# Optimization experiments

Hardware: AMD Instinct MI355X
Metric: run time of the kernel (lower is better)

## Reference

```python
import jax, jax.numpy as jnp
import numpy as np

IN_DIM = 256
OUT_DIM = 64
N = 8192
ALPHA = 0.2  # LeakyReLU negative slope
NEG_BIG = -9e15


def setup_inputs() -> dict:
    key = jax.random.key(0)
    k_h, k_A, k_W, k_a = jax.random.split(key, 4)
    h = jax.random.normal(k_h, (N, IN_DIM), dtype=jnp.float32)
    A = jax.random.randint(k_A, (N, N), 0, 2, dtype=jnp.int32)
    # xavier_uniform with gain=1.414
    gain = 1.414
    lim_W = gain * np.sqrt(6.0 / (IN_DIM + OUT_DIM))
    W = jax.random.uniform(k_W, (IN_DIM, OUT_DIM), minval=-lim_W, maxval=lim_W, dtype=jnp.float32)
    lim_a = gain * np.sqrt(6.0 / (2 * OUT_DIM + 1))
    a = jax.random.uniform(k_a, (2 * OUT_DIM, 1), minval=-lim_a, maxval=lim_a, dtype=jnp.float32)
    return {"h": h, "A": A, "W": W, "a": a}


def reference(h, A, W, a):
    # Wh: [N, d]
    Wh = h @ W
    # e_ij = leakyrelu([Wh_i || Wh_j] . a) = leakyrelu(Wh_i.a1 + Wh_j.a2)
    # -> avoid the O(N^2 * 2d) concat; compute rank-1 decomposition directly.
    a1 = a[:OUT_DIM, 0]   # [d]
    a2 = a[OUT_DIM:, 0]   # [d]
    f1 = Wh @ a1          # [N] contribution of source node i
    f2 = Wh @ a2          # [N] contribution of target node j
    e = jax.nn.leaky_relu(f1[:, None] + f2[None, :], negative_slope=ALPHA)  # [N, N]
    e = jnp.where(A > 0, e, NEG_BIG)
    attention = jax.nn.softmax(e, axis=1)  # [N, N]
    # dropout=0.0 (eval mode): identity
    h_prime = attention @ Wh               # [N, d]
    return jax.nn.elu(h_prime)             # concat=True -> ELU
```

## Files before the change

kernel.cpp:

```cpp
#include <hip/hip_runtime.h>
#include <math.h>
#include <stdint.h>

#define NV 8192
#define KD 256
#define DD 64
#define ALPHA 0.2f
#define TI 64
#define SPLIT 8
#define BLK 256

typedef _Float16 half8 __attribute__((ext_vector_type(8)));
typedef float floatx4 __attribute__((ext_vector_type(4)));

#define OFF_WHT  0
#define OFF_F1   (DD * NV / 2)
#define OFF_F2   (OFF_F1 + NV)
#define OFF_PACC (OFF_F2 + NV)

__global__ __launch_bounds__(256) void gat_pre(
    const float* __restrict__ h, const float* __restrict__ W,
    const float* __restrict__ a, ushort* __restrict__ whT,
    float* __restrict__ f1, float* __restrict__ f2) {
  __shared__ float hrow[16][KD];
  __shared__ ushort tw[DD][20];
  const int tid = threadIdx.x;
  const int i0 = blockIdx.x * 16;
#pragma unroll
  for (int u = 0; u < 4; ++u) {
    const int idx = tid + u * 256;
    const int row = idx >> 6, col = (idx & 63) * 4;
    *(float4*)&hrow[row][col] = *(const float4*)&h[(long long)(i0 + row) * KD + col];
  }
  __syncthreads();
  const int d = tid & 63;
  const int rg = tid >> 6;
  float wh[4] = {0.f, 0.f, 0.f, 0.f};
#pragma unroll 4
  for (int c = 0; c < KD; ++c) {
    const float wc = W[c * DD + d];
#pragma unroll
    for (int r = 0; r < 4; ++r) wh[r] += hrow[rg * 4 + r][c] * wc;
  }
  const float a1 = a[d], a2 = a[DD + d];
#pragma unroll
  for (int r = 0; r < 4; ++r) {
    float p1 = wh[r] * a1, p2 = wh[r] * a2;
#pragma unroll
    for (int off = 32; off > 0; off >>= 1) {
      p1 += __shfl_down(p1, off);
      p2 += __shfl_down(p2, off);
    }
    if (d == 0) { f1[i0 + rg * 4 + r] = p1; f2[i0 + rg * 4 + r] = p2; }
    union { _Float16 hf; ushort u; } cv;
    cv.hf = (_Float16)wh[r];
    tw[d][rg * 4 + r] = cv.u;
  }
  __syncthreads();
  if (tid < 128) {
    const int dd = tid >> 1, hf = tid & 1;
    *(uint4*)&whT[(long long)dd * NV + i0 + hf * 8] = *(uint4*)&tw[dd][hf * 8];
  }
}

__global__ __launch_bounds__(BLK) __attribute__((amdgpu_waves_per_eu(4, 8)))
void gat_main(
    const int* __restrict__ A, const ushort* __restrict__ whT,
    const float* __restrict__ f1, const float* __restrict__ f2,
    float* __restrict__ pacc, float* __restrict__ pl, int S) {
  __shared__ float f2_lds[NV / SPLIT];
  __shared__ float redf[4];

  const int tid = threadIdx.x;
  const int wave = tid >> 6, lane = tid & 63;
  const int m_ = lane & 15, quad = lane >> 4;
  const int tile = blockIdx.x & 127;
  const int s = blockIdx.x >> 7;
  const int i0 = tile * TI;
  const int jrange = NV / S;
  const int j0 = s * jrange;

  float m = -1e30f;
#pragma unroll
  for (int q = 0; q < NV / BLK; ++q) m = fmaxf(m, f2[tid + q * BLK]);
#pragma unroll
  for (int off = 32; off > 0; off >>= 1) m = fmaxf(m, __shfl_down(m, off));
  if (lane == 0) redf[wave] = m;

  for (int u = tid * 4; u < jrange; u += BLK * 4)
    *(float4*)&f2_lds[u] = *(const float4*)&f2[j0 + u];
  __syncthreads();

  const float mm = fmaxf(fmaxf(redf[0], redf[1]), fmaxf(redf[2], redf[3]));
  const int row = i0 + wave * 16 + m_;
  const float f1r = f1[row];
  const float xm = f1r + mm;
  const float Mr = fmaxf(xm, ALPHA * xm);

  floatx4 acc[4];
#pragma unroll
  for (int nt = 0; nt < 4; ++nt) acc[nt] = (floatx4){0.f, 0.f, 0.f, 0.f};
  float lp = 0.f;

  const int* Arow = A + (long long)row * NV + j0 + quad * 8;
  const ushort* Bb = whT + j0 + quad * 8;

  int4 aC0 = *(const int4*)(Arow);
  int4 aC1 = *(const int4*)(Arow + 4);
  half8 bC[4];
#pragma unroll
  for (int nt = 0; nt < 4; ++nt)
    bC[nt] = *(const half8*)(Bb + (long long)(nt * 16 + m_) * NV);

  for (int kb = 0; kb < jrange; kb += 32) {
    const int nxt = (kb + 32 < jrange) ? kb + 32 : 0;
    int4 aN0 = *(const int4*)(Arow + nxt);
    int4 aN1 = *(const int4*)(Arow + nxt + 4);
    half8 bN[4];
#pragma unroll
    for (int nt = 0; nt < 4; ++nt)
      bN[nt] = *(const half8*)(Bb + (long long)(nt * 16 + m_) * NV + nxt);

    const int kk = kb + quad * 8;
    const float4 q0 = *(const float4*)&f2_lds[kk];
    const float4 q1 = *(const float4*)&f2_lds[kk + 4];

    union { _Float16 hf[8]; half8 v; } wf;
#define WELT(slot, aval, f2val)                                        \
    { float x = f1r + (f2val); x = fmaxf(x, ALPHA * x);                \
      float w = ((aval) > 0) ? __expf(x - Mr) : 0.f;                   \
      wf.hf[slot] = (_Float16)w; lp += (float)wf.hf[slot]; }
    WELT(0, aC0.x, q0.x) WELT(1, aC0.y, q0.y)
    WELT(2, aC0.z, q0.z) WELT(3, aC0.w, q0.w)
    WELT(4, aC1.x, q1.x) WELT(5, aC1.y, q1.y)
    WELT(6, aC1.z, q1.z) WELT(7, aC1.w, q1.w)
#undef WELT

    acc[0] = __builtin_amdgcn_mfma_f32_16x16x32_f16(wf.v, bC[0], acc[0], 0, 0, 0);
    acc[1] = __builtin_amdgcn_mfma_f32_16x16x32_f16(wf.v, bC[1], acc[1], 0, 0, 0);
    acc[2] = __builtin_amdgcn_mfma_f32_16x16x32_f16(wf.v, bC[2], acc[2], 0, 0, 0);
    acc[3] = __builtin_amdgcn_mfma_f32_16x16x32_f16(wf.v, bC[3], acc[3], 0, 0, 0);

    aC0 = aN0; aC1 = aN1;
#pragma unroll
    for (int nt = 0; nt < 4; ++nt) bC[nt] = bN[nt];
  }

  {
    float v = lp;
    v += __shfl_down(v, 32);
    v += __shfl_down(v, 16);
    if (lane < 16) pl[(long long)s * NV + row] = v;
  }

#pragma unroll
  for (int reg = 0; reg < 4; ++reg) {
    const int i = i0 + wave * 16 + quad * 4 + reg;
    const long long base = ((long long)s * NV + i) * DD + m_;
#pragma unroll
    for (int nt = 0; nt < 4; ++nt) pacc[base + 16 * nt] = acc[nt][reg];
  }
}

__global__ __launch_bounds__(256) void gat_fin(const float* __restrict__ pacc,
                                               const float* __restrict__ pl,
                                               float* __restrict__ out, int S) {
  const int idx = blockIdx.x * 256 + threadIdx.x;
  const int i = idx >> 6;
  float sum = 0.f, l = 0.f;
  for (int q = 0; q < S; ++q) sum += pacc[(long long)q * (NV * DD) + idx];
  for (int q = 0; q < S; ++q) l += pl[q * NV + i];
  const float v = sum / l;
  out[idx] = v > 0.f ? v : expm1f(v);
}

extern "C" void kernel_launch(void* const* d_in, const int* in_sizes, int n_in,
                              void* d_out, int out_size, void* d_ws, size_t ws_size,
                              hipStream_t stream) {
  const float* h = (const float*)d_in[0];
  const int* A = (const int*)d_in[1];
  const float* W = (const float*)d_in[2];
  const float* a = (const float*)d_in[3];
  float* out = (float*)d_out;
  float* ws = (float*)d_ws;

  ushort* whT = (ushort*)(ws + OFF_WHT);
  float* f1 = ws + OFF_F1;
  float* f2 = ws + OFF_F2;
  float* pacc = ws + OFF_PACC;

  const int S = SPLIT;
  float* pl = pacc + (size_t)S * NV * DD;

  gat_pre<<<NV / 16, 256, 0, stream>>>(h, W, a, whT, f1, f2);
  gat_main<<<(NV / TI) * S, BLK, 0, stream>>>(A, whT, f1, f2, pacc, pl, S);
  gat_fin<<<NV * DD / 256, 256, 0, stream>>>(pacc, pl, out, S);
}
```

Measured before the change: 456.9 us.

## Compute softmax row sums via extra MFMA with ones, drop register prefetch, raise split

Replaces the per-element scalar accumulation of the softmax denominator with an extra MFMA against a vector of ones, which takes float adds and a cross-lane shuffle reduction off the VALU. It also removes the manual one-iteration-ahead register prefetch of A and Wh tiles, loading them directly each iteration instead. The split-K factor goes from 8 to 16 for more parallelism. The cost is larger partial buffers and more work in the final reduction, and possibly exposed load latency without the prefetch.

```diff
diff --git a/kernel.cpp b/kernel.cpp
--- a/kernel.cpp
+++ b/kernel.cpp
@@ -7,7 +7,7 @@
 #define DD 64
 #define ALPHA 0.2f
 #define TI 64
-#define SPLIT 8
+#define SPLIT 16
 #define BLK 256
 
 typedef _Float16 half8 __attribute__((ext_vector_type(8)));
@@ -97,29 +97,23 @@
   const float xm = f1r + mm;
   const float Mr = fmaxf(xm, ALPHA * xm);
 
-  floatx4 acc[4];
+  floatx4 acc[4], accl;
 #pragma unroll
   for (int nt = 0; nt < 4; ++nt) acc[nt] = (floatx4){0.f, 0.f, 0.f, 0.f};
-  float lp = 0.f;
+  accl = (floatx4){0.f, 0.f, 0.f, 0.f};
+  const half8 ones = {(_Float16)1.f, (_Float16)1.f, (_Float16)1.f, (_Float16)1.f,
+                      (_Float16)1.f, (_Float16)1.f, (_Float16)1.f, (_Float16)1.f};
 
   const int* Arow = A + (long long)row * NV + j0 + quad * 8;
   const ushort* Bb = whT + j0 + quad * 8;
 
-  int4 aC0 = *(const int4*)(Arow);
-  int4 aC1 = *(const int4*)(Arow + 4);
-  half8 bC[4];
-#pragma unroll
-  for (int nt = 0; nt < 4; ++nt)
-    bC[nt] = *(const half8*)(Bb + (long long)(nt * 16 + m_) * NV);
-
   for (int kb = 0; kb < jrange; kb += 32) {
-    const int nxt = (kb + 32 < jrange) ? kb + 32 : 0;
-    int4 aN0 = *(const int4*)(Arow + nxt);
-    int4 aN1 = *(const int4*)(Arow + nxt + 4);
-    half8 bN[4];
-#pragma unroll
-    for (int nt = 0; nt < 4; ++nt)
-      bN[nt] = *(const half8*)(Bb + (long long)(nt * 16 + m_) * NV + nxt);
+    const int4 a0 = *(const int4*)(Arow + kb);
+    const int4 a1 = *(const int4*)(Arow + kb + 4);
+    half8 b0 = *(const half8*)(Bb + (long long)(0 * 16 + m_) * NV + kb);
+    half8 b1 = *(const half8*)(Bb + (long long)(1 * 16 + m_) * NV + kb);
+    half8 b2 = *(const half8*)(Bb + (long long)(2 * 16 + m_) * NV + kb);
+    half8 b3 = *(const half8*)(Bb + (long long)(3 * 16 + m_) * NV + kb);
 
     const int kk = kb + quad * 8;
     const float4 q0 = *(const float4*)&f2_lds[kk];
@@ -129,28 +123,24 @@
 #define WELT(slot, aval, f2val)                                        \
     { float x = f1r + (f2val); x = fmaxf(x, ALPHA * x);                \
       float w = ((aval) > 0) ? __expf(x - Mr) : 0.f;                   \
-      wf.hf[slot] = (_Float16)w; lp += (float)wf.hf[slot]; }
-    WELT(0, aC0.x, q0.x) WELT(1, aC0.y, q0.y)
-    WELT(2, aC0.z, q0.z) WELT(3, aC0.w, q0.w)
-    WELT(4, aC1.x, q1.x) WELT(5, aC1.y, q1.y)
-    WELT(6, aC1.z, q1.z) WELT(7, aC1.w, q1.w)
+      wf.hf[slot] = (_Float16)w; }
+    WELT(0, a0.x, q0.x) WELT(1, a0.y, q0.y)
+    WELT(2, a0.z, q0.z) WELT(3, a0.w, q0.w)
+    WELT(4, a1.x, q1.x) WELT(5, a1.y, q1.y)
+    WELT(6, a1.z, q1.z) WELT(7, a1.w, q1.w)
 #undef WELT
 
-    acc[0] = __builtin_amdgcn_mfma_f32_16x16x32_f16(wf.v, bC[0], acc[0], 0, 0, 0);
-    acc[1] = __builtin_amdgcn_mfma_f32_16x16x32_f16(wf.v, bC[1], acc[1], 0, 0, 0);
-    acc[2] = __builtin_amdgcn_mfma_f32_16x16x32_f16(wf.v, bC[2], acc[2], 0, 0, 0);
-    acc[3] = __builtin_amdgcn_mfma_f32_16x16x32_f16(wf.v, bC[3], acc[3], 0, 0, 0);
-
-    aC0 = aN0; aC1 = aN1;
-#pragma unroll
-    for (int nt = 0; nt < 4; ++nt) bC[nt] = bN[nt];
+    acc[0] = __builtin_amdgcn_mfma_f32_16x16x32_f16(wf.v, b0, acc[0], 0, 0, 0);
+    acc[1] = __builtin_amdgcn_mfma_f32_16x16x32_f16(wf.v, b1, acc[1], 0, 0, 0);
+    acc[2] = __builtin_amdgcn_mfma_f32_16x16x32_f16(wf.v, b2, acc[2], 0, 0, 0);
+    acc[3] = __builtin_amdgcn_mfma_f32_16x16x32_f16(wf.v, b3, acc[3], 0, 0, 0);
+    accl   = __builtin_amdgcn_mfma_f32_16x16x32_f16(wf.v, ones, accl, 0, 0, 0);
   }
 
-  {
-    float v = lp;
-    v += __shfl_down(v, 32);
-    v += __shfl_down(v, 16);
-    if (lane < 16) pl[(long long)s * NV + row] = v;
+  if (m_ == 0) {
+#pragma unroll
+    for (int reg = 0; reg < 4; ++reg)
+      pl[(long long)s * NV + i0 + wave * 16 + quad * 4 + reg] = accl[reg];
   }
 
 #pragma unroll
```

After: 450.3 us. About the same (-1.4%).
